# Kernel optimization log

Hardware: AMD Instinct MI355X
Metric: run time of the kernel (lower is better)

The kernel has to match this reference:

```python
import jax, jax.numpy as jnp
import numpy as np

N, S, C, K, V = 8, 8192, 1, 1024, 64  # batch, samples, n_channels, n_classes, vec_len


def setup_inputs() -> dict:
    key = jax.random.key(0)
    k1, k2 = jax.random.split(key)
    x0 = jax.random.normal(k1, (N, S, C, V), dtype=jnp.float32)
    embedding0 = jax.random.normal(k2, (C, K, V), dtype=jnp.float32) * 0.001
    return {"x0": x0, "embedding0": embedding0}


def reference(x0, embedding0):
    # normalize=False path of the original module
    x = x0
    emb = embedding0
    Ns = x.shape[0] * x.shape[1]
    xf = x.reshape(Ns, C, V)  # (Ns, C, V)
    # squared distances ||x - e||^2 without materializing (Ns, C, K, V)
    d2 = (
        jnp.sum(xf * xf, axis=-1)[:, :, None]
        - 2.0 * jnp.einsum("ncv,ckv->nck", xf, emb)
        + jnp.sum(emb * emb, axis=-1)[None, :, :]
    )
    index = jnp.argmin(d2, axis=2)  # (Ns, C); argmin of dist == argmin of dist^2
    # histogram entropy (matches torch histc over bins 0..K-1, divided by len(index)=Ns)
    counts = jnp.zeros((K,), jnp.float32).at[index.reshape(-1)].add(1.0)
    prob = counts / Ns
    safe_log = jnp.log(jnp.where(counts > 0, prob, 1.0))
    entropy = -jnp.sum(jnp.where(counts > 0, prob * safe_log, 0.0))
    # gather codewords: embedding[c, index[n,c]]
    output = emb[jnp.arange(C)[None, :], index].reshape(x.shape)
    out0 = jax.lax.stop_gradient(output - x) + x  # straight-through
    out1 = jnp.sum((jax.lax.stop_gradient(x) - output) ** 2, axis=-1)  # (N,S,C)
    out2 = jnp.sum((x - jax.lax.stop_gradient(output)) ** 2, axis=-1)  # (N,S,C)
    return (out0, out1, out2, entropy)
```

## Files before the change

### kernel.cpp

```cpp
#include <hip/hip_runtime.h>
#include <math.h>

#define NS   65536
#define KK   1024
#define VV   64
#define SPB  128
#define NB   (NS / SPB)
#define NW   8
#define TPW  4
#define NPASS 2

#define OUT0_OFF 0
#define OUT1_OFF 4194304
#define OUT2_OFF 4259840
#define ENT_OFF  4325376


typedef __attribute__((ext_vector_type(8))) short bf16x8;
typedef __attribute__((ext_vector_type(4))) float f32x4;

__device__ __forceinline__ short f2bf(float f) {
    unsigned u = __float_as_uint(f);
    u = (u + 0x7fffu + ((u >> 16) & 1u)) >> 16;
    return (short)u;
}

__global__ void vq_prep(const float* __restrict__ emb, unsigned int* __restrict__ hist,
                        float* __restrict__ cinit, short* __restrict__ cb,
                        unsigned int* __restrict__ entCnt) {
    int t = blockIdx.x * blockDim.x + threadIdx.x;
    if (t == 0) entCnt[0] = 0u;
    if (t < KK) {
        hist[t] = 0u;
        const float4* e4 = (const float4*)(emb + (size_t)t * VV);
        const int T = t >> 4, cc = t & 15;
        float s = 0.f;
        union { short sh[8]; bf16x8 v; } pk;
        #pragma unroll
        for (int g = 0; g < 8; ++g) {
            float4 f0 = e4[2 * g], f1 = e4[2 * g + 1];
            s = fmaf(f0.x, f0.x, s); s = fmaf(f0.y, f0.y, s);
            s = fmaf(f0.z, f0.z, s); s = fmaf(f0.w, f0.w, s);
            s = fmaf(f1.x, f1.x, s); s = fmaf(f1.y, f1.y, s);
            s = fmaf(f1.z, f1.z, s); s = fmaf(f1.w, f1.w, s);
            pk.sh[0] = f2bf(f0.x); pk.sh[1] = f2bf(f0.y);
            pk.sh[2] = f2bf(f0.z); pk.sh[3] = f2bf(f0.w);
            pk.sh[4] = f2bf(f1.x); pk.sh[5] = f2bf(f1.y);
            pk.sh[6] = f2bf(f1.z); pk.sh[7] = f2bf(f1.w);
            short* dst = cb + (size_t)T * 1024 + (g >> 2) * 512 + ((g & 3) * 16 + cc) * 8;
            *(bf16x8*)dst = pk.v;
        }
        cinit[t] = 1.0f - 0.5f * s;
    }
}

__global__ __launch_bounds__(512, 4) void vq_main(
    const float* __restrict__ x, const float* __restrict__ emb,
    const float* __restrict__ cinit, const short* __restrict__ cb,
    unsigned int* __restrict__ hist,
    float* __restrict__ out0, float* __restrict__ out1, float* __restrict__ out2,
    float* __restrict__ entOut)
{
    __shared__ __align__(16) char  sA[SPB * 128];
    __shared__ float    sXn[SPB];
    __shared__ unsigned sRed[SPB][NW + 1];
    __shared__ unsigned sPkF[SPB];
    __shared__ float    sPart[NW];
    __shared__ unsigned sLast;

    const int tid  = threadIdx.x;
    const int lane = tid & 63;
    const int wv   = tid >> 6;
    const int col  = lane & 15;
    const int quad = lane >> 4;
    const int samp0 = blockIdx.x * SPB;

    {
        const int s = tid >> 2, q = tid & 3;
        const float4* xp = (const float4*)(x + (size_t)(samp0 + s) * VV + q * 16);
        float4 f0 = xp[0], f1 = xp[1], f2 = xp[2], f3 = xp[3];
        float sm = 0.f;
        sm=fmaf(f0.x,f0.x,sm); sm=fmaf(f0.y,f0.y,sm); sm=fmaf(f0.z,f0.z,sm); sm=fmaf(f0.w,f0.w,sm);
        sm=fmaf(f1.x,f1.x,sm); sm=fmaf(f1.y,f1.y,sm); sm=fmaf(f1.z,f1.z,sm); sm=fmaf(f1.w,f1.w,sm);
        sm=fmaf(f2.x,f2.x,sm); sm=fmaf(f2.y,f2.y,sm); sm=fmaf(f2.z,f2.z,sm); sm=fmaf(f2.w,f2.w,sm);
        sm=fmaf(f3.x,f3.x,sm); sm=fmaf(f3.y,f3.y,sm); sm=fmaf(f3.z,f3.z,sm); sm=fmaf(f3.w,f3.w,sm);
        union { short sh[8]; bf16x8 v; } pa, pb;
        pa.sh[0]=f2bf(f0.x); pa.sh[1]=f2bf(f0.y); pa.sh[2]=f2bf(f0.z); pa.sh[3]=f2bf(f0.w);
        pa.sh[4]=f2bf(f1.x); pa.sh[5]=f2bf(f1.y); pa.sh[6]=f2bf(f1.z); pa.sh[7]=f2bf(f1.w);
        pb.sh[0]=f2bf(f2.x); pb.sh[1]=f2bf(f2.y); pb.sh[2]=f2bf(f2.z); pb.sh[3]=f2bf(f2.w);
        pb.sh[4]=f2bf(f3.x); pb.sh[5]=f2bf(f3.y); pb.sh[6]=f2bf(f3.z); pb.sh[7]=f2bf(f3.w);
        short* base = (short*)(sA + s * 128);
        *(bf16x8*)(base + ((((2*q)    ) ^ (s & 7)) << 3)) = pa.v;
        *(bf16x8*)(base + ((((2*q) + 1) ^ (s & 7)) << 3)) = pb.v;
        sm += __shfl_xor(sm, 1, 64);
        sm += __shfl_xor(sm, 2, 64);
        if ((tid & 3) == 0) sXn[s] = sm;
    }

    const int rb0 = col * 128 + (( quad      ^ (col & 7)) << 4);
    const int rb1 = col * 128 + (((4 + quad) ^ (col & 7)) << 4);

    unsigned pmv[8];
    #pragma unroll
    for (int j = 0; j < 8; ++j) pmv[j] = 0u;

    for (int p = 0; p < NPASS; ++p) {
        bf16x8   af0[TPW], af1[TPW];
        f32x4    cv[TPW];
        unsigned inv[TPW][4];
        const int Tb = p * 32 + wv * TPW;
        #pragma unroll
        for (int t = 0; t < TPW; ++t) {
            const char* cp = (const char*)cb + (size_t)(Tb + t) * 2048;
            af0[t] = *(const bf16x8*)(cp + lane * 16);
            af1[t] = *(const bf16x8*)(cp + 1024 + lane * 16);
            cv[t]  = *(const f32x4*)(cinit + (Tb + t) * 16 + quad * 4);
            const unsigned ib = 1023u - (unsigned)((Tb + t) * 16 + quad * 4);
            inv[t][0] = ib; inv[t][1] = ib - 1; inv[t][2] = ib - 2; inv[t][3] = ib - 3;
        }
        if (p == 0) __syncthreads();

        #pragma unroll
        for (int mt = 0; mt < 8; ++mt) {
            const char* Bp = sA + mt * 2048;
            bf16x8 b0 = *(const bf16x8*)(Bp + rb0);
            bf16x8 b1 = *(const bf16x8*)(Bp + rb1);
            #pragma unroll
            for (int t = 0; t < TPW; ++t) {
                f32x4 acc = __builtin_amdgcn_mfma_f32_16x16x32_bf16(af0[t], b0, cv[t], 0, 0, 0);
                acc       = __builtin_amdgcn_mfma_f32_16x16x32_bf16(af1[t], b1, acc,   0, 0, 0);
                unsigned u0 = (__float_as_uint(acc[0]) & 0xFFFFFC00u) | inv[t][0];
                unsigned u1 = (__float_as_uint(acc[1]) & 0xFFFFFC00u) | inv[t][1];
                unsigned u2 = (__float_as_uint(acc[2]) & 0xFFFFFC00u) | inv[t][2];
                unsigned u3 = (__float_as_uint(acc[3]) & 0xFFFFFC00u) | inv[t][3];
                unsigned m0 = u0 > u1 ? u0 : u1;
                unsigned m1 = u2 > u3 ? u2 : u3;
                unsigned mm = m0 > m1 ? m0 : m1;
                pmv[mt] = pmv[mt] > mm ? pmv[mt] : mm;
            }
        }
    }

    #pragma unroll
    for (int j = 0; j < 8; ++j) {
        unsigned o;
        o = (unsigned)__shfl_xor((int)pmv[j], 16, 64); pmv[j] = o > pmv[j] ? o : pmv[j];
        o = (unsigned)__shfl_xor((int)pmv[j], 32, 64); pmv[j] = o > pmv[j] ? o : pmv[j];
    }
    {
        unsigned w0 = (quad & 1) ? pmv[1] : pmv[0];
        unsigned w1 = (quad & 1) ? pmv[3] : pmv[2];
        unsigned lo = (quad & 2) ? w1 : w0;
        unsigned w2 = (quad & 1) ? pmv[5] : pmv[4];
        unsigned w3 = (quad & 1) ? pmv[7] : pmv[6];
        unsigned hi = (quad & 2) ? w3 : w2;
        sRed[quad * 16 + col][wv]       = lo;
        sRed[(quad + 4) * 16 + col][wv] = hi;
    }
    __syncthreads();

    if (tid < SPB) {
        unsigned pbest = sRed[tid][0];
        #pragma unroll
        for (int w = 1; w < NW; ++w) {
            unsigned o = sRed[tid][w];
            pbest = o > pbest ? o : pbest;
        }
        sPkF[tid] = pbest;
        int   code = 1023 - (int)(pbest & 1023u);
        float sf   = __uint_as_float(pbest & 0xFFFFFC00u);
        float d    = fmaf(-2.f, sf - 1.0f, sXn[tid]);
        int n = samp0 + tid;
        out1[n] = d;
        out2[n] = d;
        atomicAdd(&hist[code], 1u);
    }
    __syncthreads();

    {
        float4* dstB = (float4*)(out0 + (size_t)samp0 * VV);
        #pragma unroll
        for (int i = 0; i < 4; ++i) {
            const int idx  = i * 512 + tid;
            const int smp  = idx >> 4;
            const int part = idx & 15;
            const int code = 1023 - (int)(sPkF[smp] & 1023u);
            dstB[idx] = *((const float4*)(emb + (size_t)code * VV) + part);
        }
    }

    __syncthreads();
    unsigned int* entCnt = (unsigned int*)entOut;
    if (tid == 0)
        sLast = (__hip_atomic_fetch_add(entCnt, 1u, __ATOMIC_ACQ_REL,
                                        __HIP_MEMORY_SCOPE_AGENT) == (NB - 1)) ? 1u : 0u;
    __syncthreads();
    if (sLast) {
        float e = 0.f;
        #pragma unroll
        for (int i = 0; i < 2; ++i) {
            unsigned c = __hip_atomic_load(&hist[i * 512 + tid], __ATOMIC_RELAXED,
                                           __HIP_MEMORY_SCOPE_AGENT);
            if (c) { float pr = (float)c * (1.0f / (float)NS); e -= pr * logf(pr); }
        }
        #pragma unroll
        for (int off = 32; off > 0; off >>= 1) e += __shfl_down(e, off, 64);
        if (lane == 0) sPart[wv] = e;
        __syncthreads();
        if (tid == 0) {
            float s = 0.f;
            #pragma unroll
            for (int i = 0; i < NW; ++i) s += sPart[i];
            entOut[0] = s;
        }
    }
}

extern "C" void kernel_launch(void* const* d_in, const int* in_sizes, int n_in,
                              void* d_out, int out_size, void* d_ws, size_t ws_size,
                              hipStream_t stream) {
    const float* x   = (const float*)d_in[0];
    const float* emb = (const float*)d_in[1];
    float* out = (float*)d_out;
    unsigned int* hist  = (unsigned int*)d_ws;
    float*        cinit = (float*)((char*)d_ws + 4096);
    short*        cb    = (short*)((char*)d_ws + 8192);

    vq_prep<<<4, 256, 0, stream>>>(emb, hist, cinit, cb, (unsigned int*)(out + ENT_OFF));
    vq_main<<<NB, 512, 0, stream>>>(x, emb, cinit, cb, hist,
                                    out + OUT0_OFF, out + OUT1_OFF, out + OUT2_OFF,
                                    out + ENT_OFF);
}
```

Before: 106.7 us.

## Give each wave its own samples and stream full codebook, removing LDS and block syncs

The work split changes. Before, each block's 8 waves shared 128 samples staged in LDS and each wave covered a slice of the codebook, with the slices merged through a cross-wave LDS reduction. Now each wave owns 32 samples held in registers and loops over all 64 codeword tiles, streaming them from global memory or cache. This removes shared-memory staging, the cross-wave argmin reduction and most __syncthreads, and the gather uses shuffles instead. In exchange, every wave re-reads the whole bf16 codebook (128KB), which adds cache/L2 traffic, and blocks shrink to 256 threads.

After: 133.5 us. +25.1%, slower.

```diff
diff --git a/kernel.cpp b/kernel.cpp
--- a/kernel.cpp
+++ b/kernel.cpp
@@ -4,11 +4,11 @@
 #define NS   65536
 #define KK   1024
 #define VV   64
-#define SPB  128
+#define WPB  4
+#define SPW  32
+#define SPB  (WPB * SPW)
 #define NB   (NS / SPB)
-#define NW   8
-#define TPW  4
-#define NPASS 2
+#define NT   64
 
 #define OUT0_OFF 0
 #define OUT1_OFF 4194304
@@ -54,18 +54,14 @@
     }
 }
 
-__global__ __launch_bounds__(512, 4) void vq_main(
+__global__ __launch_bounds__(256, 4) void vq_main(
     const float* __restrict__ x, const float* __restrict__ emb,
     const float* __restrict__ cinit, const short* __restrict__ cb,
     unsigned int* __restrict__ hist,
     float* __restrict__ out0, float* __restrict__ out1, float* __restrict__ out2,
     float* __restrict__ entOut)
 {
-    __shared__ __align__(16) char  sA[SPB * 128];
-    __shared__ float    sXn[SPB];
-    __shared__ unsigned sRed[SPB][NW + 1];
-    __shared__ unsigned sPkF[SPB];
-    __shared__ float    sPart[NW];
+    __shared__ float    sPart[WPB];
     __shared__ unsigned sLast;
 
     const int tid  = threadIdx.x;
@@ -73,119 +69,97 @@
     const int wv   = tid >> 6;
     const int col  = lane & 15;
     const int quad = lane >> 4;
-    const int samp0 = blockIdx.x * SPB;
-
+    const int samp0w = blockIdx.x * SPB + wv * SPW;
+
+    bf16x8 b00, b01, b10, b11;
+    float xn0, xn1;
     {
-        const int s = tid >> 2, q = tid & 3;
-        const float4* xp = (const float4*)(x + (size_t)(samp0 + s) * VV + q * 16);
-        float4 f0 = xp[0], f1 = xp[1], f2 = xp[2], f3 = xp[3];
-        float sm = 0.f;
-        sm=fmaf(f0.x,f0.x,sm); sm=fmaf(f0.y,f0.y,sm); sm=fmaf(f0.z,f0.z,sm); sm=fmaf(f0.w,f0.w,sm);
-        sm=fmaf(f1.x,f1.x,sm); sm=fmaf(f1.y,f1.y,sm); sm=fmaf(f1.z,f1.z,sm); sm=fmaf(f1.w,f1.w,sm);
-        sm=fmaf(f2.x,f2.x,sm); sm=fmaf(f2.y,f2.y,sm); sm=fmaf(f2.z,f2.z,sm); sm=fmaf(f2.w,f2.w,sm);
-        sm=fmaf(f3.x,f3.x,sm); sm=fmaf(f3.y,f3.y,sm); sm=fmaf(f3.z,f3.z,sm); sm=fmaf(f3.w,f3.w,sm);
-        union { short sh[8]; bf16x8 v; } pa, pb;
-        pa.sh[0]=f2bf(f0.x); pa.sh[1]=f2bf(f0.y); pa.sh[2]=f2bf(f0.z); pa.sh[3]=f2bf(f0.w);
-        pa.sh[4]=f2bf(f1.x); pa.sh[5]=f2bf(f1.y); pa.sh[6]=f2bf(f1.z); pa.sh[7]=f2bf(f1.w);
-        pb.sh[0]=f2bf(f2.x); pb.sh[1]=f2bf(f2.y); pb.sh[2]=f2bf(f2.z); pb.sh[3]=f2bf(f2.w);
-        pb.sh[4]=f2bf(f3.x); pb.sh[5]=f2bf(f3.y); pb.sh[6]=f2bf(f3.z); pb.sh[7]=f2bf(f3.w);
-        short* base = (short*)(sA + s * 128);
-        *(bf16x8*)(base + ((((2*q)    ) ^ (s & 7)) << 3)) = pa.v;
-        *(bf16x8*)(base + ((((2*q) + 1) ^ (s & 7)) << 3)) = pb.v;
-        sm += __shfl_xor(sm, 1, 64);
-        sm += __shfl_xor(sm, 2, 64);
-        if ((tid & 3) == 0) sXn[s] = sm;
-    }
-
-    const int rb0 = col * 128 + (( quad      ^ (col & 7)) << 4);
-    const int rb1 = col * 128 + (((4 + quad) ^ (col & 7)) << 4);
-
-    unsigned pmv[8];
-    #pragma unroll
-    for (int j = 0; j < 8; ++j) pmv[j] = 0u;
-
-    for (int p = 0; p < NPASS; ++p) {
-        bf16x8   af0[TPW], af1[TPW];
-        f32x4    cv[TPW];
-        unsigned inv[TPW][4];
-        const int Tb = p * 32 + wv * TPW;
-        #pragma unroll
-        for (int t = 0; t < TPW; ++t) {
-            const char* cp = (const char*)cb + (size_t)(Tb + t) * 2048;
-            af0[t] = *(const bf16x8*)(cp + lane * 16);
-            af1[t] = *(const bf16x8*)(cp + 1024 + lane * 16);
-            cv[t]  = *(const f32x4*)(cinit + (Tb + t) * 16 + quad * 4);
-            const unsigned ib = 1023u - (unsigned)((Tb + t) * 16 + quad * 4);
-            inv[t][0] = ib; inv[t][1] = ib - 1; inv[t][2] = ib - 2; inv[t][3] = ib - 3;
-        }
-        if (p == 0) __syncthreads();
-
-        #pragma unroll
-        for (int mt = 0; mt < 8; ++mt) {
-            const char* Bp = sA + mt * 2048;
-            bf16x8 b0 = *(const bf16x8*)(Bp + rb0);
-            bf16x8 b1 = *(const bf16x8*)(Bp + rb1);
+        const float* xw = x + (size_t)samp0w * VV;
+        #pragma unroll
+        for (int st = 0; st < 2; ++st) {
+            float s = 0.f;
+            bf16x8 vlo, vhi;
             #pragma unroll
-            for (int t = 0; t < TPW; ++t) {
-                f32x4 acc = __builtin_amdgcn_mfma_f32_16x16x32_bf16(af0[t], b0, cv[t], 0, 0, 0);
-                acc       = __builtin_amdgcn_mfma_f32_16x16x32_bf16(af1[t], b1, acc,   0, 0, 0);
-                unsigned u0 = (__float_as_uint(acc[0]) & 0xFFFFFC00u) | inv[t][0];
-                unsigned u1 = (__float_as_uint(acc[1]) & 0xFFFFFC00u) | inv[t][1];
-                unsigned u2 = (__float_as_uint(acc[2]) & 0xFFFFFC00u) | inv[t][2];
-                unsigned u3 = (__float_as_uint(acc[3]) & 0xFFFFFC00u) | inv[t][3];
-                unsigned m0 = u0 > u1 ? u0 : u1;
-                unsigned m1 = u2 > u3 ? u2 : u3;
-                unsigned mm = m0 > m1 ? m0 : m1;
-                pmv[mt] = pmv[mt] > mm ? pmv[mt] : mm;
+            for (int hf = 0; hf < 2; ++hf) {
+                const float* xp = xw + (st * 16 + col) * VV + hf * 32 + quad * 8;
+                float4 p0 = *(const float4*)(xp);
+                float4 p1 = *(const float4*)(xp + 4);
+                bf16x8 v;
+                v[0]=f2bf(p0.x); v[1]=f2bf(p0.y); v[2]=f2bf(p0.z); v[3]=f2bf(p0.w);
+                v[4]=f2bf(p1.x); v[5]=f2bf(p1.y); v[6]=f2bf(p1.z); v[7]=f2bf(p1.w);
+                s=fmaf(p0.x,p0.x,s); s=fmaf(p0.y,p0.y,s); s=fmaf(p0.z,p0.z,s); s=fmaf(p0.w,p0.w,s);
+                s=fmaf(p1.x,p1.x,s); s=fmaf(p1.y,p1.y,s); s=fmaf(p1.z,p1.z,s); s=fmaf(p1.w,p1.w,s);
+                if (hf == 0) vlo = v; else vhi = v;
             }
-        }
-    }
-
-    #pragma unroll
-    for (int j = 0; j < 8; ++j) {
+            s += __shfl_xor(s, 16, 64);
+            s += __shfl_xor(s, 32, 64);
+            if (st == 0) { b00 = vlo; b01 = vhi; xn0 = s; }
+            else         { b10 = vlo; b11 = vhi; xn1 = s; }
+        }
+    }
+
+    unsigned pm0 = 0u, pm1 = 0u;
+    const char* cbl = (const char*)cb + lane * 16;
+    const unsigned tagq = 1023u - (unsigned)(quad * 4);
+
+    #pragma unroll 8
+    for (int T = 0; T < NT; ++T) {
+        bf16x8 A0 = *(const bf16x8*)(cbl + T * 2048);
+        bf16x8 A1 = *(const bf16x8*)(cbl + T * 2048 + 1024);
+        f32x4  cv = *(const f32x4*)(cinit + T * 16 + quad * 4);
+        const unsigned tg = tagq - (unsigned)(T * 16);
+        f32x4 a0 = __builtin_amdgcn_mfma_f32_16x16x32_bf16(A0, b00, cv, 0, 0, 0);
+        a0       = __builtin_amdgcn_mfma_f32_16x16x32_bf16(A1, b01, a0, 0, 0, 0);
+        f32x4 a1 = __builtin_amdgcn_mfma_f32_16x16x32_bf16(A0, b10, cv, 0, 0, 0);
+        a1       = __builtin_amdgcn_mfma_f32_16x16x32_bf16(A1, b11, a1, 0, 0, 0);
+        unsigned u0 = (__float_as_uint(a0[0]) & 0xFFFFFC00u) | tg;
+        unsigned u1 = (__float_as_uint(a0[1]) & 0xFFFFFC00u) | (tg - 1u);
+        unsigned u2 = (__float_as_uint(a0[2]) & 0xFFFFFC00u) | (tg - 2u);
+        unsigned u3 = (__float_as_uint(a0[3]) & 0xFFFFFC00u) | (tg - 3u);
+        unsigned m0 = u0 > u1 ? u0 : u1, m1 = u2 > u3 ? u2 : u3;
+        unsigned mm = m0 > m1 ? m0 : m1;
+        pm0 = pm0 > mm ? pm0 : mm;
+        u0 = (__float_as_uint(a1[0]) & 0xFFFFFC00u) | tg;
+        u1 = (__float_as_uint(a1[1]) & 0xFFFFFC00u) | (tg - 1u);
+        u2 = (__float_as_uint(a1[2]) & 0xFFFFFC00u) | (tg - 2u);
+        u3 = (__float_as_uint(a1[3]) & 0xFFFFFC00u) | (tg - 3u);
+        m0 = u0 > u1 ? u0 : u1; m1 = u2 > u3 ? u2 : u3;
+        mm = m0 > m1 ? m0 : m1;
+        pm1 = pm1 > mm ? pm1 : mm;
+    }
+
+    {
         unsigned o;
-        o = (unsigned)__shfl_xor((int)pmv[j], 16, 64); pmv[j] = o > pmv[j] ? o : pmv[j];
-        o = (unsigned)__shfl_xor((int)pmv[j], 32, 64); pmv[j] = o > pmv[j] ? o : pmv[j];
-    }
-    {
-        unsigned w0 = (quad & 1) ? pmv[1] : pmv[0];
-        unsigned w1 = (quad & 1) ? pmv[3] : pmv[2];
-        unsigned lo = (quad & 2) ? w1 : w0;
-        unsigned w2 = (quad & 1) ? pmv[5] : pmv[4];
-        unsigned w3 = (quad & 1) ? pmv[7] : pmv[6];
-        unsigned hi = (quad & 2) ? w3 : w2;
-        sRed[quad * 16 + col][wv]       = lo;
-        sRed[(quad + 4) * 16 + col][wv] = hi;
-    }
-    __syncthreads();
-
-    if (tid < SPB) {
-        unsigned pbest = sRed[tid][0];
-        #pragma unroll
-        for (int w = 1; w < NW; ++w) {
-            unsigned o = sRed[tid][w];
-            pbest = o > pbest ? o : pbest;
-        }
-        sPkF[tid] = pbest;
-        int   code = 1023 - (int)(pbest & 1023u);
-        float sf   = __uint_as_float(pbest & 0xFFFFFC00u);
-        float d    = fmaf(-2.f, sf - 1.0f, sXn[tid]);
-        int n = samp0 + tid;
+        o = (unsigned)__shfl_xor((int)pm0, 16, 64); pm0 = o > pm0 ? o : pm0;
+        o = (unsigned)__shfl_xor((int)pm0, 32, 64); pm0 = o > pm0 ? o : pm0;
+        o = (unsigned)__shfl_xor((int)pm1, 16, 64); pm1 = o > pm1 ? o : pm1;
+        o = (unsigned)__shfl_xor((int)pm1, 32, 64); pm1 = o > pm1 ? o : pm1;
+    }
+
+    if (quad < 2) {
+        const unsigned p = quad ? pm1 : pm0;
+        const float    xnv = quad ? xn1 : xn0;
+        const int   code = 1023 - (int)(p & 1023u);
+        const float sf   = __uint_as_float(p & 0xFFFFFC00u);
+        const float d    = fmaf(-2.f, sf - 1.0f, xnv);
+        const int n = samp0w + quad * 16 + col;
         out1[n] = d;
         out2[n] = d;
         atomicAdd(&hist[code], 1u);
     }
-    __syncthreads();
 
     {
-        float4* dstB = (float4*)(out0 + (size_t)samp0 * VV);
-        #pragma unroll
-        for (int i = 0; i < 4; ++i) {
-            const int idx  = i * 512 + tid;
-            const int smp  = idx >> 4;
-            const int part = idx & 15;
-            const int code = 1023 - (int)(sPkF[smp] & 1023u);
-            dstB[idx] = *((const float4*)(emb + (size_t)code * VV) + part);
+        float4* dstW = (float4*)(out0 + (size_t)samp0w * VV);
+        #pragma unroll
+        for (int i = 0; i < 8; ++i) {
+            const int idx = i * 64 + lane;
+            const int sl  = idx >> 4;
+            const int c   = sl & 15;
+            unsigned v0 = (unsigned)__shfl((int)pm0, c, 64);
+            unsigned v1 = (unsigned)__shfl((int)pm1, c, 64);
+            unsigned p  = (sl & 16) ? v1 : v0;
+            const int code = 1023 - (int)(p & 1023u);
+            dstW[idx] = *((const float4*)(emb + (size_t)code * VV) + (idx & 15));
         }
     }
 
@@ -198,8 +172,8 @@
     if (sLast) {
         float e = 0.f;
         #pragma unroll
-        for (int i = 0; i < 2; ++i) {
-            unsigned c = __hip_atomic_load(&hist[i * 512 + tid], __ATOMIC_RELAXED,
+        for (int i = 0; i < 4; ++i) {
+            unsigned c = __hip_atomic_load(&hist[i * 256 + tid], __ATOMIC_RELAXED,
                                            __HIP_MEMORY_SCOPE_AGENT);
             if (c) { float pr = (float)c * (1.0f / (float)NS); e -= pr * logf(pr); }
         }
@@ -207,12 +181,7 @@
         for (int off = 32; off > 0; off >>= 1) e += __shfl_down(e, off, 64);
         if (lane == 0) sPart[wv] = e;
         __syncthreads();
-        if (tid == 0) {
-            float s = 0.f;
-            #pragma unroll
-            for (int i = 0; i < NW; ++i) s += sPart[i];
-            entOut[0] = s;
-        }
+        if (tid == 0) entOut[0] = sPart[0] + sPart[1] + sPart[2] + sPart[3];
     }
 }
 
@@ -227,7 +196,7 @@
     short*        cb    = (short*)((char*)d_ws + 8192);
 
     vq_prep<<<4, 256, 0, stream>>>(emb, hist, cinit, cb, (unsigned int*)(out + ENT_OFF));
-    vq_main<<<NB, 512, 0, stream>>>(x, emb, cinit, cb, hist,
+    vq_main<<<NB, 256, 0, stream>>>(x, emb, cinit, cb, hist,
                                     out + OUT0_OFF, out + OUT1_OFF, out + OUT2_OFF,
                                     out + ENT_OFF);
 }
```
